# Kernel optimization log

Measured on AMD Instinct MI355X. Metric: run time of the kernel, lower is better.

Reference implementation:

```python
import jax, jax.numpy as jnp
import numpy as np

N_HEADS = 16

def setup_inputs() -> dict:
    key = jax.random.key(0)
    ks = jax.random.split(key, 5)
    B, T, C = 4, 2048, 1024
    s = 0.02
    return {
        "x": jax.random.normal(ks[0], (B, T, C), jnp.float32),
        "W_attn": jax.random.normal(ks[1], (C, 3 * C), jnp.float32) * s,
        "b_attn": jax.random.normal(ks[2], (3 * C,), jnp.float32) * s,
        "W_proj": jax.random.normal(ks[3], (C, C), jnp.float32) * s,
        "b_proj": jax.random.normal(ks[4], (C,), jnp.float32) * s,
    }

def reference(x, W_attn, b_attn, W_proj, b_proj):
    B, T, C = x.shape
    H = N_HEADS
    D = C // H  # head dim
    qkv = x @ W_attn + b_attn                      # [B,T,3C]
    q, k, v = jnp.split(qkv, 3, axis=2)
    # [B,T,C] -> [B,H,T,D]
    q = q.reshape(B, T, H, D).transpose(0, 2, 1, 3)
    k = k.reshape(B, T, H, D).transpose(0, 2, 1, 3)
    v = v.reshape(B, T, H, D).transpose(0, 2, 1, 3)
    scale = 1.0 / jnp.sqrt(jnp.asarray(D, q.dtype))
    attn = jnp.einsum("bhqd,bhkd->bhqk", q, k) * scale  # [B,H,T,T]
    causal = jnp.tril(jnp.ones((T, T), bool))
    attn = jnp.where(causal[None, None], attn, -jnp.inf)
    attn = jax.nn.softmax(attn, axis=-1)
    y = jnp.einsum("bhqk,bhkd->bhqd", attn, v)          # [B,H,T,D]
    y = y.transpose(0, 2, 1, 3).reshape(B, T, C)
    return y @ W_proj + b_proj
```

## Files before the change

### kernel.cpp

```cpp
#include <hip/hip_runtime.h>

typedef __bf16 bf16x8 __attribute__((ext_vector_type(8)));
typedef float f32x4 __attribute__((ext_vector_type(4)));
typedef float f32x16 __attribute__((ext_vector_type(16)));
typedef unsigned short ushort8 __attribute__((ext_vector_type(8)));
typedef unsigned int uint4v __attribute__((ext_vector_type(4)));

__device__ __forceinline__ unsigned short f2bf(float f) {
  __bf16 b = (__bf16)f;
  return __builtin_bit_cast(unsigned short, b);
}
__device__ __forceinline__ float bf2f(unsigned short u) {
  unsigned int x = ((unsigned int)u) << 16;
  return __builtin_bit_cast(float, x);
}

#define GLOAD_LDS16(g, l)                                              \
  __builtin_amdgcn_global_load_lds(                                    \
      (const __attribute__((address_space(1))) void*)(g),              \
      (__attribute__((address_space(3))) void*)(l), 16, 0, 0)

__global__ __launch_bounds__(256) void f32_to_bf16_kernel(const float* __restrict__ in,
                                                          __bf16* __restrict__ out) {
  int i = blockIdx.x * 256 + threadIdx.x;
  const float4* p = (const float4*)(in + (size_t)i * 8);
  float4 f0 = p[0], f1 = p[1];
  ushort8 u = {f2bf(f0.x), f2bf(f0.y), f2bf(f0.z), f2bf(f0.w),
               f2bf(f1.x), f2bf(f1.y), f2bf(f1.z), f2bf(f1.w)};
  *(ushort8*)((unsigned short*)out + (size_t)i * 8) = u;
}

__global__ __launch_bounds__(256) void wtrans_kernel(const float* __restrict__ W,
                                                     __bf16* __restrict__ Wt,
                                                     int K, int N) {
  __shared__ float tile[32][33];
  int tx = threadIdx.x, ty = threadIdx.y;
  int n0 = blockIdx.x * 32, k0 = blockIdx.y * 32;
#pragma unroll
  for (int i = 0; i < 32; i += 8)
    tile[ty + i][tx] = W[(size_t)(k0 + ty + i) * N + n0 + tx];
  __syncthreads();
#pragma unroll
  for (int i = 0; i < 32; i += 8)
    Wt[(size_t)(n0 + ty + i) * K + k0 + tx] = (__bf16)tile[tx][ty + i];
}

template <int OUT_F32, int KSPLIT>
__global__ __launch_bounds__(256) void gemm_bt_kernel(const __bf16* __restrict__ Ab,
                                                      const __bf16* __restrict__ Bt,
                                                      const float* __restrict__ bias,
                                                      void* __restrict__ Cp,
                                                      __bf16* __restrict__ Kbp,
                                                      int M, int N, int K) {
  __shared__ __align__(16) unsigned short As[128 * 32];
  __shared__ __align__(16) unsigned short Bs[128 * 32];
  const int tid = threadIdx.x;
  const int lane = tid & 63;
  const int wid = tid >> 6;
  const int lr = lane & 15, lg = lane >> 4;
  const int gx = gridDim.x;
  int nwg = gx * gridDim.y;
  int bid = blockIdx.y * gx + blockIdx.x;
  if ((nwg & 7) == 0) {
    int cpx = nwg >> 3;
    bid = (bid & 7) * cpx + (bid >> 3);
  }
  const int m0 = (bid / gx) * 128, n0 = (bid % gx) * 128;
  const int wm = (wid >> 1) * 64, wn = (wid & 1) * 64;
  const int sr = tid >> 2, sc = (tid & 3) * 8;
  const unsigned short* Ag = (const unsigned short*)Ab + (size_t)(m0 + sr) * K + sc;
  const unsigned short* Bg = (const unsigned short*)Bt + (size_t)(n0 + sr) * K + sc;
  f32x4 acc[4][4] = {};
  for (int k0 = 0; k0 < K; k0 += 32) {
    GLOAD_LDS16(Ag + k0, As + tid * 8);
    GLOAD_LDS16(Ag + (size_t)64 * K + k0, As + 2048 + tid * 8);
    GLOAD_LDS16(Bg + k0, Bs + tid * 8);
    GLOAD_LDS16(Bg + (size_t)64 * K + k0, Bs + 2048 + tid * 8);
    __syncthreads();
    bf16x8 af[4], bfr[4];
#pragma unroll
    for (int i = 0; i < 4; ++i) af[i] = *(const bf16x8*)&As[(wm + i * 16 + lr) * 32 + lg * 8];
#pragma unroll
    for (int i = 0; i < 4; ++i) bfr[i] = *(const bf16x8*)&Bs[(wn + i * 16 + lr) * 32 + lg * 8];
#pragma unroll
    for (int i = 0; i < 4; ++i)
#pragma unroll
      for (int jn = 0; jn < 4; ++jn)
        acc[i][jn] = __builtin_amdgcn_mfma_f32_16x16x32_bf16(af[i], bfr[jn], acc[i][jn], 0, 0, 0);
    __syncthreads();
  }
  const bool isK = KSPLIT && (n0 >= 1024) && (n0 < 2048);
#pragma unroll
  for (int i = 0; i < 4; ++i)
#pragma unroll
    for (int jn = 0; jn < 4; ++jn)
#pragma unroll
      for (int jj = 0; jj < 4; ++jj) {
        int row = m0 + wm + i * 16 + lg * 4 + jj;
        int col = n0 + wn + jn * 16 + lr;
        float v = acc[i][jn][jj] + bias[col];
        if (OUT_F32) {
          ((float*)Cp)[(size_t)row * N + col] = v;
        } else if (isK) {
          int h = (col - 1024) >> 6, d = col & 63;
          int bq = row >> 11, t = row & 2047;
          ((unsigned short*)Kbp)[(size_t)((bq * 16 + h) * 2048 + t) * 64 + d] = f2bf(v);
        } else {
          ((unsigned short*)Cp)[(size_t)row * N + col] = f2bf(v);
        }
      }
}

__global__ __launch_bounds__(256) void vtrans_kernel(const __bf16* __restrict__ qkv,
                                                     __bf16* __restrict__ Vt) {
  __shared__ __align__(16) unsigned short tile[64][72];
  int bh = blockIdx.y, b = bh >> 4, h = bh & 15;
  int t0 = blockIdx.x * 64;
  int tid = threadIdx.x;
#pragma unroll
  for (int p = 0; p < 2; ++p) {
    int idx = p * 256 + tid;
    int r = idx >> 3, c8 = (idx & 7) * 8;
    *(ushort8*)&tile[r][c8] = *(const ushort8*)((const unsigned short*)qkv +
                                                (size_t)(b * 2048 + t0 + r) * 3072 + 2048 +
                                                h * 64 + c8);
  }
  __syncthreads();
#pragma unroll
  for (int p = 0; p < 2; ++p) {
    int idx = p * 256 + tid;
    int d = idx >> 3, c8 = (idx & 7) * 8;
    ushort8 u;
#pragma unroll
    for (int i = 0; i < 8; ++i) u[i] = tile[c8 + i][d];
    *(ushort8*)((unsigned short*)Vt + (size_t)(bh * 64 + d) * 2048 + t0 + c8) = u;
  }
}

__global__ __launch_bounds__(512) void attn_kernel(const __bf16* __restrict__ qkvp,
                                                   const __bf16* __restrict__ Kg,
                                                   const __bf16* __restrict__ Vt,
                                                   __bf16* __restrict__ yb) {
  __shared__ __align__(16) unsigned short Ks[2][64][72];
  __shared__ __align__(16) unsigned short Vs[2][64][72];
  const int bx = blockIdx.x;
  const int qb = 7 - (bx >> 6);
  const int bh = bx & 63;
  const int b = bh >> 4, h = bh & 15;
  const int tid = threadIdx.x, wid = tid >> 6, lane = tid & 63;
  const int lq = lane & 31, hi = lane >> 5;
  const unsigned short* qkv = (const unsigned short*)qkvp;
  const unsigned short* Kh = (const unsigned short*)Kg + (size_t)bh * 2048 * 64;
  const unsigned short* Vh = (const unsigned short*)Vt + (size_t)bh * 64 * 2048;
  const int q0w = qb * 256 + wid * 32;
  const int jmax_w = 4 * qb + (wid >> 1);
  const int qrel = (wid & 1) * 32 + lq;
  const int J = 4 * qb + 4;
  const int r = tid >> 3, c8s = (tid & 7) * 8;

  const float qs = 0.125f * 1.44269504f;
  bf16x8 qf[4];
  {
    const unsigned short* Qg = qkv + (size_t)(b * 2048 + q0w + lq) * 3072 + h * 64;
#pragma unroll
    for (int dc = 0; dc < 4; ++dc) {
      ushort8 uq = *(const ushort8*)(Qg + dc * 16 + hi * 8);
      uint4v w;
#pragma unroll
      for (int i = 0; i < 4; ++i) {
        float lo = bf2f(uq[2 * i]) * qs;
        float hh = bf2f(uq[2 * i + 1]) * qs;
        unsigned int up;
        asm("v_cvt_pk_bf16_f32 %0, %1, %2" : "=v"(up) : "v"(lo), "v"(hh));
        w[i] = up;
      }
      qf[dc] = __builtin_bit_cast(bf16x8, w);
    }
  }

  f32x16 yacc[2] = {};
  float m_r = -1e30f, l_r = 0.f;

  *(ushort8*)&Ks[0][r][c8s] = *(const ushort8*)(Kh + (size_t)r * 64 + c8s);
  *(ushort8*)&Vs[0][r][c8s] = *(const ushort8*)(Vh + (size_t)r * 2048 + c8s);

  for (int j = 0; j < J; ++j) {
    __syncthreads();
    if (j + 1 < J) {
      int bi = (j + 1) & 1;
      *(ushort8*)&Ks[bi][r][c8s] =
          *(const ushort8*)(Kh + (size_t)((j + 1) * 64 + r) * 64 + c8s);
      *(ushort8*)&Vs[bi][r][c8s] =
          *(const ushort8*)(Vh + (size_t)r * 2048 + (j + 1) * 64 + c8s);
    }
    if (j <= jmax_w) {
      const int cb = j & 1;
      f32x16 sa[2];
#pragma unroll
      for (int kt32 = 0; kt32 < 2; ++kt32) {
        f32x16 s = {};
#pragma unroll
        for (int dc = 0; dc < 4; ++dc) {
          bf16x8 kf = *(const bf16x8*)&Ks[cb][kt32 * 32 + lq][dc * 16 + hi * 8];
          s = __builtin_amdgcn_mfma_f32_32x32x16_bf16(kf, qf[dc], s, 0, 0, 0);
        }
        sa[kt32] = s;
      }
      if (j == jmax_w) {
#pragma unroll
        for (int kt32 = 0; kt32 < 2; ++kt32)
#pragma unroll
          for (int reg = 0; reg < 16; ++reg) {
            int kl = kt32 * 32 + (reg & 3) + 8 * (reg >> 2) + 4 * hi;
            if (kl > qrel) sa[kt32][reg] = -1e30f;
          }
      }
      float pmax = -1e30f;
#pragma unroll
      for (int kt32 = 0; kt32 < 2; ++kt32)
#pragma unroll
        for (int reg = 0; reg < 16; reg += 4)
          pmax = fmaxf(pmax, fmaxf(fmaxf(sa[kt32][reg], sa[kt32][reg + 1]),
                                   fmaxf(sa[kt32][reg + 2], sa[kt32][reg + 3])));
      pmax = fmaxf(pmax, __shfl_xor(pmax, 32));
      const bool need = __any(pmax > m_r + 8.f) != 0;
      const float mnew = need ? fmaxf(m_r, pmax) : m_r;
      const float alpha = exp2f(m_r - mnew);
      unsigned int u[2][8];
      float rs = 0.f;
#pragma unroll
      for (int kt32 = 0; kt32 < 2; ++kt32)
#pragma unroll
        for (int rr = 0; rr < 8; ++rr) {
          float p0 = exp2f(sa[kt32][2 * rr] - mnew);
          float p1 = exp2f(sa[kt32][2 * rr + 1] - mnew);
          rs += p0 + p1;
          unsigned int up;
          asm("v_cvt_pk_bf16_f32 %0, %1, %2" : "=v"(up) : "v"(p0), "v"(p1));
          u[kt32][rr] = up;
        }
      rs += __shfl_xor(rs, 32);
      l_r = l_r * alpha + rs;
      m_r = mnew;
      if (need) {
#pragma unroll
        for (int reg = 0; reg < 16; ++reg) {
          int row = (reg & 3) + 8 * (reg >> 2) + 4 * hi;
          float ac = __shfl(alpha, row);
          yacc[0][reg] *= ac;
          yacc[1][reg] *= ac;
        }
      }
#pragma unroll
      for (int kt = 0; kt < 4; ++kt) {
        const int kt32 = kt >> 1, off = 4 * (kt & 1);
        unsigned int a0 = u[kt32][off + 0], a2 = u[kt32][off + 2];
        unsigned int a1 = u[kt32][off + 1], a3 = u[kt32][off + 3];
        asm("v_permlane32_swap_b32 %0, %1" : "+v"(a0), "+v"(a2));
        asm("v_permlane32_swap_b32 %0, %1" : "+v"(a1), "+v"(a3));
        uint4v pav = {a0, a1, a2, a3};
        bf16x8 paf = __builtin_bit_cast(bf16x8, pav);
#pragma unroll
        for (int dt = 0; dt < 2; ++dt) {
          bf16x8 vf = *(const bf16x8*)&Vs[cb][dt * 32 + lq][kt * 16 + hi * 8];
          yacc[dt] = __builtin_amdgcn_mfma_f32_32x32x16_bf16(paf, vf, yacc[dt], 0, 0, 0);
        }
      }
    }
  }
#pragma unroll
  for (int reg = 0; reg < 16; ++reg) {
    int row = (reg & 3) + 8 * (reg >> 2) + 4 * hi;
    float linv = 1.f / __shfl(l_r, row);
    int qg = q0w + row;
#pragma unroll
    for (int dt = 0; dt < 2; ++dt) {
      float v = yacc[dt][reg] * linv;
      ((unsigned short*)yb)[(size_t)(b * 2048 + qg) * 1024 + h * 64 + dt * 32 + lq] = f2bf(v);
    }
  }
}

extern "C" void kernel_launch(void* const* d_in, const int* in_sizes, int n_in,
                              void* d_out, int out_size, void* d_ws, size_t ws_size,
                              hipStream_t stream) {
  const float* x = (const float*)d_in[0];
  const float* W_attn = (const float*)d_in[1];
  const float* b_attn = (const float*)d_in[2];
  const float* W_proj = (const float*)d_in[3];
  const float* b_proj = (const float*)d_in[4];
  float* out = (float*)d_out;
  char* ws = (char*)d_ws;

  size_t off = 0;
  __bf16* WtA = (__bf16*)(ws + off); off += (size_t)3072 * 1024 * 2;
  __bf16* WtP = (__bf16*)(ws + off); off += (size_t)1024 * 1024 * 2;
  __bf16* qkv = (__bf16*)(ws + off); off += (size_t)8192 * 3072 * 2;
  __bf16* Kb  = (__bf16*)(ws + off); off += (size_t)64 * 2048 * 64 * 2;
  __bf16* Vtb = (__bf16*)(ws + off); off += (size_t)64 * 2048 * 64 * 2;
  __bf16* xyb = (__bf16*)(ws + off); off += (size_t)8192 * 1024 * 2;
  __bf16* xb = xyb;
  __bf16* yb = xyb;
  (void)ws_size; (void)in_sizes; (void)n_in; (void)out_size;

  f32_to_bf16_kernel<<<4096, 256, 0, stream>>>(x, xb);
  wtrans_kernel<<<dim3(3072 / 32, 1024 / 32), dim3(32, 8), 0, stream>>>(W_attn, WtA, 1024, 3072);
  wtrans_kernel<<<dim3(1024 / 32, 1024 / 32), dim3(32, 8), 0, stream>>>(W_proj, WtP, 1024, 1024);
  gemm_bt_kernel<0, 1><<<dim3(24, 64), 256, 0, stream>>>(xb, WtA, b_attn, qkv, Kb, 8192, 3072, 1024);
  vtrans_kernel<<<dim3(32, 64), 256, 0, stream>>>(qkv, Vtb);
  attn_kernel<<<dim3(512), 512, 0, stream>>>(qkv, Kb, Vtb, yb);
  gemm_bt_kernel<1, 0><<<dim3(8, 64), 256, 0, stream>>>(yb, WtP, b_proj, out, nullptr, 8192, 1024, 1024);
}
```

Measured before the change: 202.0 us.

## Rewrite projection GEMMs with 256x128 tiles, double-buffered LDS and swizzle

Replaces the 128x128, single-buffered GEMM with a 512-thread kernel computing 256x128 tiles with a K-step of 64. Global-to-LDS loads are double-buffered and the next stage is issued while the current one runs MFMAs, using explicit vmcnt waits and barriers. LDS columns are XOR-swizzled to avoid bank conflicts, and MFMA sections raise wave priority. The aim is to hide memory latency and cut barrier overhead, at the cost of much more LDS per block (96 KB), which limits occupancy.

```diff
diff --git a/kernel.cpp b/kernel.cpp
--- a/kernel.cpp
+++ b/kernel.cpp
@@ -46,18 +46,19 @@
 }
 
 template <int OUT_F32, int KSPLIT>
-__global__ __launch_bounds__(256) void gemm_bt_kernel(const __bf16* __restrict__ Ab,
-                                                      const __bf16* __restrict__ Bt,
-                                                      const float* __restrict__ bias,
-                                                      void* __restrict__ Cp,
-                                                      __bf16* __restrict__ Kbp,
-                                                      int M, int N, int K) {
-  __shared__ __align__(16) unsigned short As[128 * 32];
-  __shared__ __align__(16) unsigned short Bs[128 * 32];
+__global__ __launch_bounds__(512, 2) void gemm256_kernel(const __bf16* __restrict__ Ab,
+                                                         const __bf16* __restrict__ Bt,
+                                                         const float* __restrict__ bias,
+                                                         void* __restrict__ Cp,
+                                                         __bf16* __restrict__ Kbp,
+                                                         int M, int N, int K) {
+  __shared__ __align__(16) unsigned short As[2][256 * 64];
+  __shared__ __align__(16) unsigned short Bs[2][128 * 64];
   const int tid = threadIdx.x;
   const int lane = tid & 63;
   const int wid = tid >> 6;
   const int lr = lane & 15, lg = lane >> 4;
+  const int wr = wid >> 1, wc = wid & 1;
   const int gx = gridDim.x;
   int nwg = gx * gridDim.y;
   int bid = blockIdx.y * gx + blockIdx.x;
@@ -65,46 +66,84 @@
     int cpx = nwg >> 3;
     bid = (bid & 7) * cpx + (bid >> 3);
   }
-  const int m0 = (bid / gx) * 128, n0 = (bid % gx) * 128;
-  const int wm = (wid >> 1) * 64, wn = (wid & 1) * 64;
-  const int sr = tid >> 2, sc = (tid & 3) * 8;
-  const unsigned short* Ag = (const unsigned short*)Ab + (size_t)(m0 + sr) * K + sc;
-  const unsigned short* Bg = (const unsigned short*)Bt + (size_t)(n0 + sr) * K + sc;
+  const int m0 = (bid / gx) * 256, n0 = (bid % gx) * 128;
+  const int srow = tid >> 3;
+  const int scol = ((tid & 7) ^ (srow & 7)) * 8;
+  const unsigned short* Ag = (const unsigned short*)Ab + (size_t)(m0 + srow) * K + scol;
+  const unsigned short* Bg = (const unsigned short*)Bt + (size_t)(n0 + srow) * K + scol;
+
+#define STAGE256(t, bi)                                                      \
+  {                                                                          \
+    const int _k0 = (t) * 64;                                                \
+    GLOAD_LDS16(Ag + _k0, &As[bi][tid * 8]);                                 \
+    GLOAD_LDS16(Ag + (size_t)64 * K + _k0, &As[bi][4096 + tid * 8]);         \
+    GLOAD_LDS16(Ag + (size_t)128 * K + _k0, &As[bi][8192 + tid * 8]);        \
+    GLOAD_LDS16(Ag + (size_t)192 * K + _k0, &As[bi][12288 + tid * 8]);       \
+    GLOAD_LDS16(Bg + _k0, &Bs[bi][tid * 8]);                                 \
+    GLOAD_LDS16(Bg + (size_t)64 * K + _k0, &Bs[bi][4096 + tid * 8]);         \
+  }
+
   f32x4 acc[4][4] = {};
-  for (int k0 = 0; k0 < K; k0 += 32) {
-    GLOAD_LDS16(Ag + k0, As + tid * 8);
-    GLOAD_LDS16(Ag + (size_t)64 * K + k0, As + 2048 + tid * 8);
-    GLOAD_LDS16(Bg + k0, Bs + tid * 8);
-    GLOAD_LDS16(Bg + (size_t)64 * K + k0, Bs + 2048 + tid * 8);
-    __syncthreads();
-    bf16x8 af[4], bfr[4];
-#pragma unroll
-    for (int i = 0; i < 4; ++i) af[i] = *(const bf16x8*)&As[(wm + i * 16 + lr) * 32 + lg * 8];
-#pragma unroll
-    for (int i = 0; i < 4; ++i) bfr[i] = *(const bf16x8*)&Bs[(wn + i * 16 + lr) * 32 + lg * 8];
-#pragma unroll
-    for (int i = 0; i < 4; ++i)
-#pragma unroll
-      for (int jn = 0; jn < 4; ++jn)
-        acc[i][jn] = __builtin_amdgcn_mfma_f32_16x16x32_bf16(af[i], bfr[jn], acc[i][jn], 0, 0, 0);
-    __syncthreads();
-  }
+  const int nst = K >> 6;
+  STAGE256(0, 0);
+  STAGE256(1, 1);
+  int aoff[4][2], boff[4][2];
+#pragma unroll
+  for (int t = 0; t < 4; ++t)
+#pragma unroll
+    for (int ks = 0; ks < 2; ++ks) {
+      int slot = ((ks * 4 + lg) ^ (lr & 7));
+      aoff[t][ks] = (wr * 64 + t * 16 + lr) * 64 + slot * 8;
+      boff[t][ks] = (wc * 64 + t * 16 + lr) * 64 + slot * 8;
+    }
+
+  for (int i = 0; i < nst; ++i) {
+    const int cur = i & 1;
+    if (i + 1 < nst)
+      asm volatile("s_waitcnt vmcnt(6)" ::: "memory");
+    else
+      asm volatile("s_waitcnt vmcnt(0)" ::: "memory");
+    asm volatile("s_barrier" ::: "memory");
+    bf16x8 af[4][2], bq[4][2];
+#pragma unroll
+    for (int t = 0; t < 4; ++t)
+#pragma unroll
+      for (int ks = 0; ks < 2; ++ks) {
+        af[t][ks] = *(const bf16x8*)&As[cur][aoff[t][ks]];
+        bq[t][ks] = *(const bf16x8*)&Bs[cur][boff[t][ks]];
+      }
+    asm volatile("s_waitcnt lgkmcnt(0)" ::: "memory");
+    asm volatile("s_barrier" ::: "memory");
+    if (i + 2 < nst) STAGE256(i + 2, cur);
+    __builtin_amdgcn_s_setprio(1);
+#pragma unroll
+    for (int mt = 0; mt < 4; ++mt)
+#pragma unroll
+      for (int nt = 0; nt < 4; ++nt)
+#pragma unroll
+        for (int ks = 0; ks < 2; ++ks)
+          acc[mt][nt] =
+              __builtin_amdgcn_mfma_f32_16x16x32_bf16(af[mt][ks], bq[nt][ks], acc[mt][nt], 0, 0, 0);
+    __builtin_amdgcn_s_setprio(0);
+  }
+#undef STAGE256
+
   const bool isK = KSPLIT && (n0 >= 1024) && (n0 < 2048);
 #pragma unroll
-  for (int i = 0; i < 4; ++i)
-#pragma unroll
-    for (int jn = 0; jn < 4; ++jn)
+  for (int mt = 0; mt < 4; ++mt)
+#pragma unroll
+    for (int nt = 0; nt < 4; ++nt)
 #pragma unroll
       for (int jj = 0; jj < 4; ++jj) {
-        int row = m0 + wm + i * 16 + lg * 4 + jj;
-        int col = n0 + wn + jn * 16 + lr;
-        float v = acc[i][jn][jj] + bias[col];
+        int row = m0 + wr * 64 + mt * 16 + lg * 4 + jj;
+        int col = n0 + wc * 64 + nt * 16 + lr;
+        float v = acc[mt][nt][jj] + bias[col];
         if (OUT_F32) {
           ((float*)Cp)[(size_t)row * N + col] = v;
         } else if (isK) {
           int h = (col - 1024) >> 6, d = col & 63;
-          int bq = row >> 11, t = row & 2047;
-          ((unsigned short*)Kbp)[(size_t)((bq * 16 + h) * 2048 + t) * 64 + d] = f2bf(v);
+          int bq2 = row >> 11, t = row & 2047;
+          ((unsigned short*)Kbp)[(size_t)((bq2 * 16 + h) * 2048 + t) * 64 + d] = f2bf(v);
         } else {
           ((unsigned short*)Cp)[(size_t)row * N + col] = f2bf(v);
         }
@@ -306,8 +345,8 @@
   f32_to_bf16_kernel<<<4096, 256, 0, stream>>>(x, xb);
   wtrans_kernel<<<dim3(3072 / 32, 1024 / 32), dim3(32, 8), 0, stream>>>(W_attn, WtA, 1024, 3072);
   wtrans_kernel<<<dim3(1024 / 32, 1024 / 32), dim3(32, 8), 0, stream>>>(W_proj, WtP, 1024, 1024);
-  gemm_bt_kernel<0, 1><<<dim3(24, 64), 256, 0, stream>>>(xb, WtA, b_attn, qkv, Kb, 8192, 3072, 1024);
+  gemm256_kernel<0, 1><<<dim3(24, 32), 512, 0, stream>>>(xb, WtA, b_attn, qkv, Kb, 8192, 3072, 1024);
   vtrans_kernel<<<dim3(32, 64), 256, 0, stream>>>(qkv, Vtb);
   attn_kernel<<<dim3(512), 512, 0, stream>>>(qkv, Kb, Vtb, yb);
-  gemm_bt_kernel<1, 0><<<dim3(8, 64), 256, 0, stream>>>(yb, WtP, b_proj, out, nullptr, 8192, 1024, 1024);
-}
+  gemm256_kernel<1, 0><<<dim3(8, 32), 512, 0, stream>>>(yb, WtP, b_proj, out, nullptr, 8192, 1024, 1024);
+}
```

Measured after the change: 192.2 us. 1.05x faster.
